# Kernel optimization log

Measured on AMD Instinct MI355X. Metric: run time of the kernel, lower is better.

The kernel has to match this reference:

```python
import jax, jax.numpy as jnp
import numpy as np

N_NODES = 50000
N_EDGES = 800000
N_GRAPHS = 512
EPS = 1e-5
SLOPE = 0.2  # LeakyReLU negative slope in GATv2


def setup_inputs() -> dict:
    key = jax.random.key(0)
    ks = jax.random.split(key, 20)
    s = 0.1
    inp = {
        "x": jax.random.normal(ks[0], (N_NODES, 9), jnp.float32),
        "edge_attr": jax.random.normal(ks[1], (N_EDGES, 3), jnp.float32),
        "Wl0": jax.random.normal(ks[2], (9, 64), jnp.float32) * s,
        "Wr0": jax.random.normal(ks[3], (9, 64), jnp.float32) * s,
        "bl0": jnp.zeros((64,), jnp.float32),
        "br0": jnp.zeros((64,), jnp.float32),
        "We0": jax.random.normal(ks[4], (3, 64), jnp.float32) * s,
        "att0": jax.random.normal(ks[5], (64,), jnp.float32) * s,
        "bo0": jnp.zeros((64,), jnp.float32),
        "Wl": jax.random.normal(ks[6], (4, 64, 64), jnp.float32) * s,
        "Wr": jax.random.normal(ks[7], (4, 64, 64), jnp.float32) * s,
        "bl": jnp.zeros((4, 64), jnp.float32),
        "br": jnp.zeros((4, 64), jnp.float32),
        "We": jax.random.normal(ks[8], (4, 3, 64), jnp.float32) * s,
        "att": jax.random.normal(ks[9], (4, 64), jnp.float32) * s,
        "bo": jnp.zeros((4, 64), jnp.float32),
        "bn_g": jnp.ones((5, 64), jnp.float32),
        "bn_b": jnp.zeros((5, 64), jnp.float32),
        "bn_m": jnp.zeros((5, 64), jnp.float32),
        "bn_v": jax.random.uniform(ks[10], (5, 64), jnp.float32, 0.5, 1.5),
        "Wjk": jax.random.normal(ks[11], (64, 64), jnp.float32) * s,
        "bjk": jnp.zeros((64,), jnp.float32),
        "Whead": jax.random.normal(ks[12], (64, 1), jnp.float32) * s,
        "bhead": jnp.zeros((1,), jnp.float32),
        "edge_index": jax.random.randint(ks[13], (2, N_EDGES), 0, N_NODES, jnp.int32),
        "batch": jnp.sort(jax.random.randint(ks[14], (N_NODES,), 0, N_GRAPHS, jnp.int32)),
        "num_graphs": N_GRAPHS,
    }
    return inp


def gatv2_layer(h, src, dst, ea, Wl_, bl_, Wr_, br_, We_, a_, bo_, n_nodes):
    # GATv2Conv (heads=1, edge_dim) : e_ij = a . LeakyReLU(Wl h_j + Wr h_i + We e_ij)
    xl = h @ Wl_ + bl_                          # [N, 64] source transform
    xr = h @ Wr_ + br_                          # [N, 64] dest transform
    e = jax.nn.leaky_relu(xl[src] + xr[dst] + ea @ We_, SLOPE)  # [E, 64]
    logit = e @ a_                              # [E]
    m = jax.ops.segment_max(logit, dst, num_segments=n_nodes)
    m = jnp.where(jnp.isfinite(m), m, 0.0)      # empty segments -> -inf
    p = jnp.exp(logit - m[dst])
    z = jax.ops.segment_sum(p, dst, num_segments=n_nodes)
    alpha = p / jnp.maximum(z[dst], 1e-16)      # softmax over in-edges of dst
    out = jax.ops.segment_sum(alpha[:, None] * xl[src], dst, num_segments=n_nodes)
    return out + bo_


def bn_relu(h, g, b, m, v):
    # eval-mode BatchNorm1d followed by ReLU (BasicGNN: norm then act)
    return jax.nn.relu((h - m) * (g * jax.lax.rsqrt(v + EPS)) + b)


def reference(x, edge_attr, Wl0, Wr0, bl0, br0, We0, att0, bo0,
              Wl, Wr, bl, br, We, att, bo,
              bn_g, bn_b, bn_m, bn_v, Wjk, bjk, Whead, bhead,
              edge_index, batch, num_graphs):
    n = x.shape[0]
    src, dst = edge_index[0], edge_index[1]
    h = gatv2_layer(x, src, dst, edge_attr, Wl0, bl0, Wr0, br0, We0, att0, bo0, n)
    h = bn_relu(h, bn_g[0], bn_b[0], bn_m[0], bn_v[0])
    for i in range(4):
        h = gatv2_layer(h, src, dst, edge_attr, Wl[i], bl[i], Wr[i], br[i], We[i], att[i], bo[i], n)
        h = bn_relu(h, bn_g[i + 1], bn_b[i + 1], bn_m[i + 1], bn_v[i + 1])
    h = h @ Wjk + bjk                            # jk='last' output projection 64->64
    # global mean pool over graphs
    sums = jax.ops.segment_sum(h, batch, num_segments=num_graphs)          # [G, 64]
    cnt = jax.ops.segment_sum(jnp.ones((n,), h.dtype), batch, num_segments=num_graphs)
    pooled = sums / jnp.maximum(cnt, 1.0)[:, None]
    return pooled @ Whead + bhead                # [G, 1]  (dropout inactive in eval)
```

## Files before the change

### kernel.cpp

```cpp
#include <hip/hip_runtime.h>
#include <math.h>

#define N_NODES 50000
#define N_EDGES 800000
#define N_GRAPHS 512
#define SLOPE 0.2f
static constexpr float EPS_BN = 1e-5f;

typedef float v2f __attribute__((ext_vector_type(2)));


__global__ void hist_kernel(const int* __restrict__ dst, int* __restrict__ cnt) {
    int e = blockIdx.x * blockDim.x + threadIdx.x;
    if (e < N_EDGES) atomicAdd(&cnt[dst[e]], 1);
}

__global__ void scan1_kernel(const int* __restrict__ cnt, int* __restrict__ row_ptr,
                             int* __restrict__ blk) {
    __shared__ int tmp[1024];
    int t = threadIdx.x;
    int n = blockIdx.x * 1024 + t;
    int v = (n < N_NODES) ? cnt[n] : 0;
    tmp[t] = v;
    __syncthreads();
    for (int off = 1; off < 1024; off <<= 1) {
        int x = (t >= off) ? tmp[t - off] : 0;
        __syncthreads();
        tmp[t] += x;
        __syncthreads();
    }
    if (n < N_NODES) row_ptr[n + 1] = tmp[t];
    if (t == 1023) blk[blockIdx.x] = tmp[t];
}

__global__ void scan23f_kernel(int* __restrict__ row_ptr, const int* __restrict__ blk,
                               int* __restrict__ fill) {
    int n = blockIdx.x * blockDim.x + threadIdx.x;
    if (n >= N_NODES) return;
    int b = n >> 10;
    int pref = 0;
    for (int i = 0; i < b; ++i) pref += blk[i];
    int v = row_ptr[n + 1] + pref;
    row_ptr[n + 1] = v;
    fill[n + 1] = v;
    if (n == 0) { row_ptr[0] = 0; fill[0] = 0; }
}

__global__ void scatter_kernel(const int* __restrict__ src, const int* __restrict__ dst,
                               const float* __restrict__ ea,
                               int* __restrict__ fill,
                               float4* __restrict__ rec) {
    int e = blockIdx.x * blockDim.x + threadIdx.x;
    if (e < N_EDGES) {
        int pos = atomicAdd(&fill[dst[e]], 1);
        rec[pos] = make_float4(__int_as_float(src[e]),
                               ea[e * 3 + 0], ea[e * 3 + 1], ea[e * 3 + 2]);
    }
}


template <int K>
__global__ __launch_bounds__(256) void transform3_kernel(
    const float* __restrict__ h,
    const float* __restrict__ Wl, const float* __restrict__ bl,
    const float* __restrict__ Wr, const float* __restrict__ br,
    float* __restrict__ xl, float* __restrict__ xr) {
    int t = threadIdx.x;
    int w = t >> 6;
    int k = t & 63;
    float wl[K], wr[K];
#pragma unroll
    for (int j = 0; j < K; j++) { wl[j] = Wl[j * 64 + k]; wr[j] = Wr[j * 64 + k]; }
    float blk = bl[k], brk = br[k];
    int wid = blockIdx.x * 4 + w;
    const int NW = gridDim.x * 4;
    for (int n = wid; n < N_NODES; n += NW) {
        int un = __builtin_amdgcn_readfirstlane(n);
        const float* __restrict__ hrow = h + (size_t)un * K;
        float al = blk, ar = brk;
#pragma unroll
        for (int j = 0; j < K; j++) {
            float hj = hrow[j];
            al = fmaf(hj, wl[j], al);
            ar = fmaf(hj, wr[j], ar);
        }
        xl[(size_t)un * 64 + k] = al;
        xr[(size_t)un * 64 + k] = ar;
    }
}


__global__ __launch_bounds__(256) void gat_fused4_kernel(
    const float* __restrict__ xl, const float* __restrict__ xr,
    const float4* __restrict__ recP, const int* __restrict__ row_ptr,
    const float* __restrict__ We, const float* __restrict__ att,
    const float* __restrict__ bo,
    const float* __restrict__ bn_g, const float* __restrict__ bn_b,
    const float* __restrict__ bn_m, const float* __restrict__ bn_v,
    float* __restrict__ hout) {
    int t = threadIdx.x;
    int w = t >> 6;
    int lane = t & 63;
    int q = lane >> 4;
    int r = lane & 15;
    int k4 = r * 4;
    int n = blockIdx.x * 4 + w;

    float4 we0 = *(const float4*)(We + 0 * 64 + k4);
    float4 we1 = *(const float4*)(We + 64 + k4);
    float4 we2 = *(const float4*)(We + 128 + k4);
    float4 at4 = *(const float4*)(att + k4);
    float4 xq  = *(const float4*)(xr + (size_t)n * 64 + k4);
    v2f we0a = {we0.x, we0.y}, we0b = {we0.z, we0.w};
    v2f we1a = {we1.x, we1.y}, we1b = {we1.z, we1.w};
    v2f we2a = {we2.x, we2.y}, we2b = {we2.z, we2.w};
    v2f ata  = {at4.x, at4.y}, atb  = {at4.z, at4.w};
    v2f xra  = {xq.x, xq.y},   xrb  = {xq.z, xq.w};
    int beg = row_ptr[n], end = row_ptr[n + 1];

    v2f oAa = {0.f, 0.f}, oAb = {0.f, 0.f};
    v2f oBa = {0.f, 0.f}, oBb = {0.f, 0.f};
    float zA = 0.f, zB = 0.f;

    for (int c = beg; c < end; c += 8) {
        int pA = c + q;     bool vA = pA < end; int iA = vA ? pA : beg;
        int pB = c + 4 + q; bool vB = pB < end; int iB = vB ? pB : beg;
        float4 rA = recP[iA];
        float4 rB = recP[iB];
        int sA = __float_as_int(rA.x);
        int sB = __float_as_int(rB.x);
        float4 xA = *(const float4*)(xl + (size_t)sA * 64 + k4);
        float4 xB = *(const float4*)(xl + (size_t)sB * 64 + k4);
        v2f xAa = {xA.x, xA.y}, xAb = {xA.z, xA.w};
        v2f xBa = {xB.x, xB.y}, xBb = {xB.z, xB.w};

        v2f tAa = xAa + xra, tAb = xAb + xrb;
        v2f tBa = xBa + xra, tBb = xBb + xrb;
        tAa = __builtin_elementwise_fma((v2f){rA.y, rA.y}, we0a, tAa);
        tAb = __builtin_elementwise_fma((v2f){rA.y, rA.y}, we0b, tAb);
        tBa = __builtin_elementwise_fma((v2f){rB.y, rB.y}, we0a, tBa);
        tBb = __builtin_elementwise_fma((v2f){rB.y, rB.y}, we0b, tBb);
        tAa = __builtin_elementwise_fma((v2f){rA.z, rA.z}, we1a, tAa);
        tAb = __builtin_elementwise_fma((v2f){rA.z, rA.z}, we1b, tAb);
        tBa = __builtin_elementwise_fma((v2f){rB.z, rB.z}, we1a, tBa);
        tBb = __builtin_elementwise_fma((v2f){rB.z, rB.z}, we1b, tBb);
        tAa = __builtin_elementwise_fma((v2f){rA.w, rA.w}, we2a, tAa);
        tAb = __builtin_elementwise_fma((v2f){rA.w, rA.w}, we2b, tAb);
        tBa = __builtin_elementwise_fma((v2f){rB.w, rB.w}, we2a, tBa);
        tBb = __builtin_elementwise_fma((v2f){rB.w, rB.w}, we2b, tBb);

        tAa = __builtin_elementwise_max(tAa, tAa * SLOPE);
        tAb = __builtin_elementwise_max(tAb, tAb * SLOPE);
        tBa = __builtin_elementwise_max(tBa, tBa * SLOPE);
        tBb = __builtin_elementwise_max(tBb, tBb * SLOPE);

        v2f dA = ata * tAa; dA = __builtin_elementwise_fma(atb, tAb, dA);
        v2f dB = ata * tBa; dB = __builtin_elementwise_fma(atb, tBb, dB);
        float accA = dA.x + dA.y;
        float accB = dB.x + dB.y;

        accA += __shfl_xor(accA, 1, 64);  accB += __shfl_xor(accB, 1, 64);
        accA += __shfl_xor(accA, 2, 64);  accB += __shfl_xor(accB, 2, 64);
        accA += __shfl_xor(accA, 4, 64);  accB += __shfl_xor(accB, 4, 64);
        accA += __shfl_xor(accA, 8, 64);  accB += __shfl_xor(accB, 8, 64);

        float peA = vA ? __expf(accA) : 0.f;
        float peB = vB ? __expf(accB) : 0.f;
        v2f pA2 = {peA, peA}, pB2 = {peB, peB};
        oAa = __builtin_elementwise_fma(pA2, xAa, oAa);
        oAb = __builtin_elementwise_fma(pA2, xAb, oAb);
        oBa = __builtin_elementwise_fma(pB2, xBa, oBa);
        oBb = __builtin_elementwise_fma(pB2, xBb, oBb);
        zA += peA; zB += peB;
    }

    v2f oa = oAa + oBa, ob = oAb + oBb;
    float z = zA + zB;
    float4 o = make_float4(oa.x, oa.y, ob.x, ob.y);
    o.x += __shfl_xor(o.x, 16, 64); o.x += __shfl_xor(o.x, 32, 64);
    o.y += __shfl_xor(o.y, 16, 64); o.y += __shfl_xor(o.y, 32, 64);
    o.z += __shfl_xor(o.z, 16, 64); o.z += __shfl_xor(o.z, 32, 64);
    o.w += __shfl_xor(o.w, 16, 64); o.w += __shfl_xor(o.w, 32, 64);
    z += __shfl_xor(z, 16, 64); z += __shfl_xor(z, 32, 64);

    if (q == 0) {
        float zi = 1.0f / fmaxf(z, 1e-16f);
        float4 bo4 = *(const float4*)(bo + k4);
        float4 g4  = *(const float4*)(bn_g + k4);
        float4 b4  = *(const float4*)(bn_b + k4);
        float4 m4  = *(const float4*)(bn_m + k4);
        float4 v4  = *(const float4*)(bn_v + k4);
        float4 res;
        res.x = fmaxf((o.x * zi + bo4.x - m4.x) * (g4.x / sqrtf(v4.x + EPS_BN)) + b4.x, 0.f);
        res.y = fmaxf((o.y * zi + bo4.y - m4.y) * (g4.y / sqrtf(v4.y + EPS_BN)) + b4.y, 0.f);
        res.z = fmaxf((o.z * zi + bo4.z - m4.z) * (g4.z / sqrtf(v4.z + EPS_BN)) + b4.z, 0.f);
        res.w = fmaxf((o.w * zi + bo4.w - m4.w) * (g4.w / sqrtf(v4.w + EPS_BN)) + b4.w, 0.f);
        *(float4*)(hout + (size_t)n * 64 + k4) = res;
    }
}


__global__ __launch_bounds__(64) void pool_all_kernel(
    const float* __restrict__ h, const int* __restrict__ batch,
    const float* __restrict__ Wjk, const float* __restrict__ bjk,
    const float* __restrict__ Whead, const float* __restrict__ bhead,
    float* __restrict__ out) {
    int g = blockIdx.x;
    int k = threadIdx.x;
    int lo = 0, hi = N_NODES;
    while (lo < hi) { int mid = (lo + hi) >> 1; if (batch[mid] < g) lo = mid + 1; else hi = mid; }
    int s = lo;
    hi = N_NODES;
    while (lo < hi) { int mid = (lo + hi) >> 1; if (batch[mid] < g + 1) lo = mid + 1; else hi = mid; }
    int e = lo;

    float wc = 0.f;
    for (int j = 0; j < 64; j++) wc = fmaf(Wjk[k * 64 + j], Whead[j], wc);
    float bc = bjk[k] * Whead[k];
    for (int off = 32; off > 0; off >>= 1) bc += __shfl_xor(bc, off, 64);

    float acc = 0.f;
    for (int n = s; n < e; ++n) acc += h[(size_t)n * 64 + k];
    float cnt = (float)(e - s);
    acc /= fmaxf(cnt, 1.0f);
    float v = acc * wc;
    for (int off = 32; off > 0; off >>= 1) v += __shfl_xor(v, off, 64);
    if (k == 0) out[g] = v + bc + bhead[0];
}


extern "C" void kernel_launch(void* const* d_in, const int* in_sizes, int n_in,
                              void* d_out, int out_size, void* d_ws, size_t ws_size,
                              hipStream_t stream) {
    const float* x     = (const float*)d_in[0];
    const float* ea    = (const float*)d_in[1];
    const float* Wl0   = (const float*)d_in[2];
    const float* Wr0   = (const float*)d_in[3];
    const float* bl0   = (const float*)d_in[4];
    const float* br0   = (const float*)d_in[5];
    const float* We0   = (const float*)d_in[6];
    const float* att0  = (const float*)d_in[7];
    const float* bo0   = (const float*)d_in[8];
    const float* Wl    = (const float*)d_in[9];
    const float* Wr    = (const float*)d_in[10];
    const float* bl    = (const float*)d_in[11];
    const float* br    = (const float*)d_in[12];
    const float* We    = (const float*)d_in[13];
    const float* att   = (const float*)d_in[14];
    const float* bo    = (const float*)d_in[15];
    const float* bn_g  = (const float*)d_in[16];
    const float* bn_b  = (const float*)d_in[17];
    const float* bn_m  = (const float*)d_in[18];
    const float* bn_v  = (const float*)d_in[19];
    const float* Wjk   = (const float*)d_in[20];
    const float* bjk   = (const float*)d_in[21];
    const float* Whead = (const float*)d_in[22];
    const float* bhead = (const float*)d_in[23];
    const int* edge_index = (const int*)d_in[24];
    const int* batch      = (const int*)d_in[25];

    const int* srcIdx = edge_index;
    const int* dstIdx = edge_index + N_EDGES;

    char* ws = (char*)d_ws;
    size_t off = 0;
    auto alloc = [&](size_t bytes) -> void* {
        void* p = ws + off;
        off += (bytes + 255) & ~(size_t)255;
        return p;
    };
    float* hA      = (float*)alloc((size_t)N_NODES * 64 * 4);
    float* hB      = (float*)alloc((size_t)N_NODES * 64 * 4);
    float* xlb     = (float*)alloc((size_t)N_NODES * 64 * 4);
    float* xrb     = (float*)alloc((size_t)N_NODES * 64 * 4);
    int*   row_ptr = (int*)alloc((size_t)(N_NODES + 1) * 4);
    int*   fill    = (int*)alloc((size_t)(N_NODES + 1) * 4);
    int*   blk     = (int*)alloc(64 * 4);
    float4* recP   = (float4*)alloc((size_t)N_EDGES * 16);

    hipMemsetAsync(fill, 0, (size_t)N_NODES * 4, stream);
    hist_kernel<<<(N_EDGES + 255) / 256, 256, 0, stream>>>(dstIdx, fill);
    const int SCB = (N_NODES + 1023) / 1024;
    scan1_kernel<<<SCB, 1024, 0, stream>>>(fill, row_ptr, blk);
    scan23f_kernel<<<(N_NODES + 255) / 256, 256, 0, stream>>>(row_ptr, blk, fill);
    scatter_kernel<<<(N_EDGES + 255) / 256, 256, 0, stream>>>(srcIdx, dstIdx, ea, fill, recP);

    const int NBN = N_NODES / 4;
    const int NBT = 768;

    transform3_kernel<9><<<NBT, 256, 0, stream>>>(x, Wl0, bl0, Wr0, br0, xlb, xrb);
    gat_fused4_kernel<<<NBN, 256, 0, stream>>>(xlb, xrb, recP, row_ptr,
                                               We0, att0, bo0,
                                               bn_g, bn_b, bn_m, bn_v, hA);

    float* hcur = hA;
    float* hnext = hB;
    for (int i = 0; i < 4; i++) {
        transform3_kernel<64><<<NBT, 256, 0, stream>>>(hcur,
            Wl + (size_t)i * 64 * 64, bl + (size_t)i * 64,
            Wr + (size_t)i * 64 * 64, br + (size_t)i * 64,
            xlb, xrb);
        gat_fused4_kernel<<<NBN, 256, 0, stream>>>(xlb, xrb, recP, row_ptr,
            We + (size_t)i * 3 * 64, att + (size_t)i * 64,
            bo + (size_t)i * 64,
            bn_g + (size_t)(i + 1) * 64, bn_b + (size_t)(i + 1) * 64,
            bn_m + (size_t)(i + 1) * 64, bn_v + (size_t)(i + 1) * 64,
            hnext);
        float* tp = hcur; hcur = hnext; hnext = tp;
    }

    pool_all_kernel<<<N_GRAPHS, 64, 0, stream>>>(hcur, batch, Wjk, bjk, Whead, bhead,
                                                 (float*)d_out);
}
```

Before: 553.0 us.

## Replace per-node GEMV transform with LDS-tiled register-blocked GEMM for hidden layers

The 64-wide layer transform now stages a 64-node tile of h (transposed) and the concatenated Wl|Wr weights in shared memory, then has each thread compute a 4x8 output block using packed v2f FMAs. This replaces the previous one-node-per-wavefront GEMV, which re-read h rows through scalar loads and held 128 weight values in registers. The first layer gets a packed-FMA variant of the old kernel with a different grid size. The costs are higher LDS use per block (about 50 KB) and possible bank conflicts on the transposed writes.

```diff
diff --git a/kernel.cpp b/kernel.cpp
--- a/kernel.cpp
+++ b/kernel.cpp
@@ -59,8 +59,7 @@
 }
 
 
-template <int K>
-__global__ __launch_bounds__(256) void transform3_kernel(
+__global__ __launch_bounds__(256) void transform9_kernel(
     const float* __restrict__ h,
     const float* __restrict__ Wl, const float* __restrict__ bl,
     const float* __restrict__ Wr, const float* __restrict__ br,
@@ -68,24 +67,113 @@
     int t = threadIdx.x;
     int w = t >> 6;
     int k = t & 63;
-    float wl[K], wr[K];
-#pragma unroll
-    for (int j = 0; j < K; j++) { wl[j] = Wl[j * 64 + k]; wr[j] = Wr[j * 64 + k]; }
-    float blk = bl[k], brk = br[k];
+    v2f wlr[9];
+#pragma unroll
+    for (int j = 0; j < 9; j++) wlr[j] = (v2f){Wl[j * 64 + k], Wr[j * 64 + k]};
+    v2f bias = {bl[k], br[k]};
     int wid = blockIdx.x * 4 + w;
     const int NW = gridDim.x * 4;
     for (int n = wid; n < N_NODES; n += NW) {
         int un = __builtin_amdgcn_readfirstlane(n);
-        const float* __restrict__ hrow = h + (size_t)un * K;
-        float al = blk, ar = brk;
-#pragma unroll
-        for (int j = 0; j < K; j++) {
-            float hj = hrow[j];
-            al = fmaf(hj, wl[j], al);
-            ar = fmaf(hj, wr[j], ar);
+        const float* __restrict__ hrow = h + (size_t)un * 9;
+        float hb[9];
+#pragma unroll
+        for (int j = 0; j < 9; j++) hb[j] = hrow[j];
+        v2f acc = bias;
+#pragma unroll
+        for (int j = 0; j < 9; j++)
+            acc = __builtin_elementwise_fma((v2f){hb[j], hb[j]}, wlr[j], acc);
+        xl[(size_t)un * 64 + k] = acc.x;
+        xr[(size_t)un * 64 + k] = acc.y;
+    }
+}
+
+
+__global__ __launch_bounds__(256) void transform5_kernel(
+    const float* __restrict__ h,
+    const float* __restrict__ Wl, const float* __restrict__ bl,
+    const float* __restrict__ Wr, const float* __restrict__ br,
+    float* __restrict__ xl, float* __restrict__ xr) {
+    __shared__ float sAt[64][68];
+    __shared__ float sB[64][128];
+    int t = threadIdx.x;
+    int n0 = blockIdx.x * 64;
+
+#pragma unroll
+    for (int i = 0; i < 4; i++) {
+        int idx = i * 256 + t;
+        int row = idx >> 4;
+        int fc  = idx & 15;
+        int n = n0 + row;
+        float4 v = (n < N_NODES) ? *((const float4*)(h + (size_t)n * 64 + fc * 4))
+                                 : make_float4(0.f, 0.f, 0.f, 0.f);
+        sAt[fc * 4 + 0][row] = v.x;
+        sAt[fc * 4 + 1][row] = v.y;
+        sAt[fc * 4 + 2][row] = v.z;
+        sAt[fc * 4 + 3][row] = v.w;
+    }
+#pragma unroll
+    for (int i = 0; i < 8; i++) {
+        int idx = i * 256 + t;
+        int j  = idx >> 5;
+        int fc = idx & 31;
+        int c  = fc * 4;
+        float4 v = (c < 64) ? *((const float4*)(Wl + j * 64 + c))
+                            : *((const float4*)(Wr + j * 64 + (c - 64)));
+        *((float4*)&sB[j][c]) = v;
+    }
+    __syncthreads();
+
+    int tx = t & 15, ty = t >> 4;
+    int col0 = tx * 8;
+    const float* bsrc = (col0 < 64) ? (bl + col0) : (br + (col0 - 64));
+    v2f acc[4][4];
+#pragma unroll
+    for (int r = 0; r < 4; r++)
+#pragma unroll
+        for (int cc = 0; cc < 4; cc++)
+            acc[r][cc] = (v2f){bsrc[cc * 2], bsrc[cc * 2 + 1]};
+
+#pragma unroll 4
+    for (int j = 0; j < 64; j++) {
+        float a0 = sAt[j][ty * 4 + 0];
+        float a1 = sAt[j][ty * 4 + 1];
+        float a2 = sAt[j][ty * 4 + 2];
+        float a3 = sAt[j][ty * 4 + 3];
+        float4 bq0 = *((const float4*)&sB[j][col0]);
+        float4 bq1 = *((const float4*)&sB[j][col0 + 4]);
+        v2f b0 = {bq0.x, bq0.y}, b1 = {bq0.z, bq0.w};
+        v2f b2 = {bq1.x, bq1.y}, b3 = {bq1.z, bq1.w};
+        v2f a0v = {a0, a0}, a1v = {a1, a1}, a2v = {a2, a2}, a3v = {a3, a3};
+        acc[0][0] = __builtin_elementwise_fma(a0v, b0, acc[0][0]);
+        acc[0][1] = __builtin_elementwise_fma(a0v, b1, acc[0][1]);
+        acc[0][2] = __builtin_elementwise_fma(a0v, b2, acc[0][2]);
+        acc[0][3] = __builtin_elementwise_fma(a0v, b3, acc[0][3]);
+        acc[1][0] = __builtin_elementwise_fma(a1v, b0, acc[1][0]);
+        acc[1][1] = __builtin_elementwise_fma(a1v, b1, acc[1][1]);
+        acc[1][2] = __builtin_elementwise_fma(a1v, b2, acc[1][2]);
+        acc[1][3] = __builtin_elementwise_fma(a1v, b3, acc[1][3]);
+        acc[2][0] = __builtin_elementwise_fma(a2v, b0, acc[2][0]);
+        acc[2][1] = __builtin_elementwise_fma(a2v, b1, acc[2][1]);
+        acc[2][2] = __builtin_elementwise_fma(a2v, b2, acc[2][2]);
+        acc[2][3] = __builtin_elementwise_fma(a2v, b3, acc[2][3]);
+        acc[3][0] = __builtin_elementwise_fma(a3v, b0, acc[3][0]);
+        acc[3][1] = __builtin_elementwise_fma(a3v, b1, acc[3][1]);
+        acc[3][2] = __builtin_elementwise_fma(a3v, b2, acc[3][2]);
+        acc[3][3] = __builtin_elementwise_fma(a3v, b3, acc[3][3]);
+    }
+
+#pragma unroll
+    for (int r = 0; r < 4; r++) {
+        int n = n0 + ty * 4 + r;
+        if (n < N_NODES) {
+            float4 lo = make_float4(acc[r][0].x, acc[r][0].y, acc[r][1].x, acc[r][1].y);
+            float4 hi = make_float4(acc[r][2].x, acc[r][2].y, acc[r][3].x, acc[r][3].y);
+            float* dst = (col0 < 64) ? (xl + (size_t)n * 64 + col0)
+                                     : (xr + (size_t)n * 64 + (col0 - 64));
+            *((float4*)dst) = lo;
+            *((float4*)(dst + 4)) = hi;
         }
-        xl[(size_t)un * 64 + k] = al;
-        xr[(size_t)un * 64 + k] = ar;
     }
 }
 
@@ -286,9 +374,9 @@
     scatter_kernel<<<(N_EDGES + 255) / 256, 256, 0, stream>>>(srcIdx, dstIdx, ea, fill, recP);
 
     const int NBN = N_NODES / 4;
-    const int NBT = 768;
-
-    transform3_kernel<9><<<NBT, 256, 0, stream>>>(x, Wl0, bl0, Wr0, br0, xlb, xrb);
+    const int NBG = (N_NODES + 63) / 64;
+
+    transform9_kernel<<<512, 256, 0, stream>>>(x, Wl0, bl0, Wr0, br0, xlb, xrb);
     gat_fused4_kernel<<<NBN, 256, 0, stream>>>(xlb, xrb, recP, row_ptr,
                                                We0, att0, bo0,
                                                bn_g, bn_b, bn_m, bn_v, hA);
@@ -296,7 +384,7 @@
     float* hcur = hA;
     float* hnext = hB;
     for (int i = 0; i < 4; i++) {
-        transform3_kernel<64><<<NBT, 256, 0, stream>>>(hcur,
+        transform5_kernel<<<NBG, 256, 0, stream>>>(hcur,
             Wl + (size_t)i * 64 * 64, bl + (size_t)i * 64,
             Wr + (size_t)i * 64 * 64, br + (size_t)i * 64,
             xlb, xrb);
```

Result: no change. 554.9 us (+0.3%).
